# Kernel tuning notes

Measured on AMD Instinct MI355X. Metric: run time of the kernel, lower is better.

## Reference

```python
import jax, jax.numpy as jnp
import numpy as np

N = 30000      # input points
M = 7500       # sampled queries = floor(N * ratio), ratio=0.25
K = 16         # neighbors per query
D_X = 64       # input feature dim
D_REL = 64     # point_pos_nn output dim
D_F = D_X + D_REL  # fij_hat dim = 128


def setup_inputs() -> dict:
    key = jax.random.key(0)
    ks = jax.random.split(key, 6)
    x = jax.random.normal(ks[0], (N, D_X), jnp.float32)
    pos = jax.random.normal(ks[1], (N, 3), jnp.float32)
    idx = jax.random.randint(ks[2], (M,), 0, N)
    W_pos = jax.random.normal(ks[3], (10, D_REL), jnp.float32) / jnp.sqrt(10.0)
    b_pos = jnp.zeros((D_REL,), jnp.float32)
    W_att = jax.random.normal(ks[4], (D_F, D_F), jnp.float32) / jnp.sqrt(float(D_F))
    b_att = jnp.zeros((D_F,), jnp.float32)
    W_glob = jax.random.normal(ks[5], (D_F, D_F), jnp.float32) / jnp.sqrt(float(D_F))
    b_glob = jnp.zeros((D_F,), jnp.float32)
    return {"x": x, "pos": pos, "idx": idx, "W_pos": W_pos, "b_pos": b_pos,
            "W_att": W_att, "b_att": b_att, "W_glob": W_glob, "b_glob": b_glob}


def reference(x, pos, idx, W_pos, b_pos, W_att, b_att, W_glob, b_glob):
    # --- KNN: brute-force squared distances from sampled queries to all points ---
    pos_q = pos[idx]                                         # [M, 3]
    d2 = ((pos_q * pos_q).sum(-1)[:, None]
          + (pos * pos).sum(-1)[None, :]
          - 2.0 * pos_q @ pos.T)                             # [M, N]
    _, nbr = jax.lax.top_k(-d2, K)                           # [M, K] neighbor indices

    # --- Local Spatial Encoding (message) ---
    pos_j = pos[nbr]                                         # [M, K, 3]
    pos_i = jnp.broadcast_to(pos_q[:, None, :], pos_j.shape) # [M, K, 3]
    vij = pos_i - pos_j                                      # [M, K, 3]
    dij = jnp.linalg.norm(vij, axis=-1, keepdims=True)       # [M, K, 1]
    rel = jnp.concatenate([pos_i, pos_j, vij, dij], axis=-1) # [M, K, 10]
    rij = jax.nn.relu(rel @ W_pos + b_pos)                   # [M, K, D_REL]

    # --- Attentive pooling ---
    fij = jnp.concatenate([x[nbr], rij], axis=-1)            # [M, K, D_F]
    g = fij @ W_att + b_att                                  # [M, K, D_F]
    s = jax.nn.softmax(g, axis=-1)                           # softmax over feature dim
    aggr = jnp.mean(s * fij, axis=1)                         # mean over K neighbors -> [M, D_F]

    # --- global_nn (update) ---
    return jax.nn.relu(aggr @ W_glob + b_glob)               # [M, D_F]
```

## Files before the change

kernel.cpp:

```cpp
#include <hip/hip_runtime.h>
#include <stdint.h>

#define KNB   16
#define GD    64
#define GTOT  (GD * GD * GD)
#define GORIG (-6.5f)
#define GEDGE 0.203125f
#define GINV  (1.0f / GEDGE)
#define CAPW  640

typedef short short8 __attribute__((ext_vector_type(8)));
typedef float floatx4 __attribute__((ext_vector_type(4)));

__device__ __forceinline__ unsigned short f2bf(float x) {
  union { float f; uint32_t u; } v; v.f = x;
  uint32_t u = v.u + 0x7FFFu + ((v.u >> 16) & 1u);
  return (unsigned short)(u >> 16);
}
__device__ __forceinline__ float bf2f(unsigned short b) {
  return __uint_as_float(((uint32_t)b) << 16);
}
__device__ __forceinline__ int cellco(float v) {
  int c = (int)floorf((v - GORIG) * GINV);
  return c < 0 ? 0 : (c > GD - 1 ? GD - 1 : c);
}

__global__ void zero_kernel(int* __restrict__ count) {
  int i = (blockIdx.x * 256 + threadIdx.x) * 4;
  *(int4*)(count + i) = make_int4(0, 0, 0, 0);
}

__global__ void prep_kernel(const float* __restrict__ x,
                            const float* __restrict__ pos,
                            const float* __restrict__ W_att,
                            unsigned short* __restrict__ xb,
                            float4* __restrict__ pos4,
                            unsigned short* __restrict__ Wt,
                            int* __restrict__ ptcell,
                            int* __restrict__ count, int N) {
  int id = blockIdx.x * 256 + threadIdx.x;
  int nx8 = N * 8;
  if (id < nx8) {
    const float4* src = (const float4*)x + (size_t)id * 2;
    float4 a = src[0], b = src[1];
    short8 v;
    v[0] = (short)f2bf(a.x); v[1] = (short)f2bf(a.y);
    v[2] = (short)f2bf(a.z); v[3] = (short)f2bf(a.w);
    v[4] = (short)f2bf(b.x); v[5] = (short)f2bf(b.y);
    v[6] = (short)f2bf(b.z); v[7] = (short)f2bf(b.w);
    *(short8*)(xb + (size_t)id * 8) = v;
  } else if (id < nx8 + N) {
    int j = id - nx8;
    float px = pos[3 * j], py = pos[3 * j + 1], pz = pos[3 * j + 2];
    float pp = fmaf(px, px, fmaf(py, py, pz * pz));
    pos4[j] = make_float4(px, py, pz, pp);
    int cid = (cellco(pz) * GD + cellco(py)) * GD + cellco(px);
    ptcell[j] = cid;
    atomicAdd(&count[cid], 1);
  } else if (id < nx8 + N + 128 * 128) {
    int t = id - nx8 - N;
    int c = t >> 7, f = t & 127;
    Wt[f * 128 + c] = f2bf(W_att[t]);
  }
}

__global__ __launch_bounds__(256) void scan1(const int* __restrict__ count,
                                             int* __restrict__ partial) {
  int b = blockIdx.x, t = threadIdx.x;
  int v = count[b * 256 + t];
#pragma unroll
  for (int off = 1; off < 64; off <<= 1) v += __shfl_xor(v, off);
  __shared__ int ws_[4];
  if ((t & 63) == 0) ws_[t >> 6] = v;
  __syncthreads();
  if (t == 0) partial[b] = ws_[0] + ws_[1] + ws_[2] + ws_[3];
}

__global__ __launch_bounds__(256) void scan2(int* __restrict__ partial,
                                             int* __restrict__ cell_start) {
  int t = threadIdx.x;
  int v0 = partial[t * 4], v1 = partial[t * 4 + 1];
  int v2 = partial[t * 4 + 2], v3 = partial[t * 4 + 3];
  int s1 = v0 + v1, s2 = s1 + v2, s3 = s2 + v3;
  int x = s3;
  int lane = t & 63, wv = t >> 6;
#pragma unroll
  for (int off = 1; off < 64; off <<= 1) {
    int y = __shfl_up(x, off);
    if (lane >= off) x += y;
  }
  __shared__ int wsum[4];
  if (lane == 63) wsum[wv] = x;
  __syncthreads();
  int base = 0;
  for (int k = 0; k < wv; ++k) base += wsum[k];
  int excl = base + x - s3;
  partial[t * 4]     = excl;
  partial[t * 4 + 1] = excl + v0;
  partial[t * 4 + 2] = excl + s1;
  partial[t * 4 + 3] = excl + s2;
  if (t == 255) cell_start[GTOT] = excl + s3;
}

__global__ __launch_bounds__(256) void scan3(const int* __restrict__ count,
                                             const int* __restrict__ partial,
                                             int* __restrict__ cell_start,
                                             int* __restrict__ cursor) {
  int b = blockIdx.x, t = threadIdx.x;
  int v = count[b * 256 + t];
  int x = v;
  int lane = t & 63, wv = t >> 6;
#pragma unroll
  for (int off = 1; off < 64; off <<= 1) {
    int y = __shfl_up(x, off);
    if (lane >= off) x += y;
  }
  __shared__ int wsum[4];
  if (lane == 63) wsum[wv] = x;
  __syncthreads();
  int base = partial[b];
  for (int k = 0; k < wv; ++k) base += wsum[k];
  int excl = base + x - v;
  cell_start[b * 256 + t] = excl;
  cursor[b * 256 + t] = excl;
}

__global__ void scatter_kernel(const float4* __restrict__ pos4,
                               const int* __restrict__ ptcell,
                               int* __restrict__ cursor,
                               float4* __restrict__ spos4,
                               int* __restrict__ sid, int N) {
  int j = blockIdx.x * 256 + threadIdx.x;
  if (j >= N) return;
  int cid = ptcell[j];
  int slot = atomicAdd(&cursor[cid], 1);
  spos4[slot] = pos4[j];
  sid[slot] = j;
}

__global__ __launch_bounds__(256) void knn_grid(
    const float4* __restrict__ pos4, const float4* __restrict__ spos4,
    const int* __restrict__ sid, const int* __restrict__ cell_start,
    const int* __restrict__ idx, int* __restrict__ nbr, int M) {
  __shared__ unsigned long long cand[4][CAPW];
  __shared__ uint32_t rsA[4][64], rlA[4][64], rsB[4][64];
  __shared__ uint32_t rps[4][72];
  const int tid = threadIdx.x, wv = tid >> 6, ln = tid & 63;
  const int m = blockIdx.x * 4 + wv;
  if (m >= M) return;

  const float4 qp = pos4[idx[m]];
  const int cqx = cellco(qp.x), cqy = cellco(qp.y), cqz = cellco(qp.z);

  int tot = 0;
  unsigned long long taukey = ~0ull;
  bool done = false;
  for (int s = 1; s <= 64 && !done; ++s) {
    const int w = 2 * s + 1, npair = w * w;
    for (int base = 0; base < npair; base += 64) {
      int i = base + ln;
      int stA = 0, lA = 0, stB = 0, lB = 0;
      if (i < npair) {
        int dz = i / w - s, dy = i - (i / w) * w - s;
        int cz = cqz + dz, cy = cqy + dy;
        if (cz >= 0 && cz < GD && cy >= 0 && cy < GD) {
          int rowbase = (cz * GD + cy) * GD;
          int az = dz < 0 ? -dz : dz, ay = dy < 0 ? -dy : dy;
          int ch = az > ay ? az : ay;
          if (s == 1 || ch == s) {
            int x0 = cqx - s; if (x0 < 0) x0 = 0;
            int x1 = cqx + s; if (x1 > GD - 1) x1 = GD - 1;
            stA = cell_start[rowbase + x0];
            lA  = cell_start[rowbase + x1 + 1] - stA;
          } else {
            int xl = cqx - s, xr = cqx + s;
            if (xl >= 0) {
              stA = cell_start[rowbase + xl];
              lA  = cell_start[rowbase + xl + 1] - stA;
            }
            if (xr <= GD - 1) {
              stB = cell_start[rowbase + xr];
              lB  = cell_start[rowbase + xr + 1] - stB;
            }
          }
        }
      }
      int len = lA + lB;
      int xinc = len;
#pragma unroll
      for (int off = 1; off < 64; off <<= 1) {
        int y = __shfl_up(xinc, off);
        if (ln >= off) xinc += y;
      }
      int T = __shfl(xinc, 63);
      if (T == 0) continue;
      rps[wv][ln] = (uint32_t)(xinc - len);
      if (ln == 63) rps[wv][64] = (uint32_t)T;
      rsA[wv][ln] = (uint32_t)stA;
      rlA[wv][ln] = (uint32_t)lA;
      rsB[wv][ln] = (uint32_t)stB;

      for (int b2 = 0; b2 < T; b2 += 64) {
        if (tot + 64 > CAPW) {
          unsigned long long c[CAPW / 64];
#pragma unroll
          for (int chk = 0; chk < CAPW / 64; ++chk) {
            int slot = chk * 64 + ln;
            c[chk] = (slot < tot) ? cand[wv][slot] : ~0ull;
          }
          unsigned long long last = 0;
#pragma unroll
          for (int r = 0; r < KNB; ++r) {
            unsigned long long mn = c[0];
#pragma unroll
            for (int chk = 1; chk < CAPW / 64; ++chk)
              mn = (c[chk] < mn) ? c[chk] : mn;
#pragma unroll
            for (int off = 1; off < 64; off <<= 1) {
              unsigned long long o = __shfl_xor(mn, off);
              mn = (o < mn) ? o : mn;
            }
            if (ln == 0) cand[wv][r] = mn;
            last = mn;
#pragma unroll
            for (int chk = 0; chk < CAPW / 64; ++chk)
              if (c[chk] == mn) c[chk] = ~0ull;
          }
          tot = KNB;
          taukey = last;
        }
        int flat = b2 + ln;
        unsigned long long key = ~0ull;
        bool ok = false;
        if (flat < T) {
          int lo = 0;
#pragma unroll
          for (int step = 32; step > 0; step >>= 1) {
            int mid = lo + step;
            if (mid <= 63 && (int)rps[wv][mid] <= flat) lo = mid;
          }
          int o = flat - (int)rps[wv][lo];
          uint32_t sa = rsA[wv][lo], la = rlA[wv][lo];
          int p = (o < (int)la) ? (int)(sa + o)
                                : (int)(rsB[wv][lo] + (uint32_t)(o - (int)la));
          float4 pj = spos4[p];
          float dot = fmaf(qp.x, pj.x, fmaf(qp.y, pj.y, qp.z * pj.z));
          float tt  = fmaf(-2.f, dot, pj.w);
          float d2  = fmaxf(qp.w + tt, 0.f);
          key = ((unsigned long long)__float_as_uint(d2) << 32) |
                (uint32_t)sid[p];
          ok = key < taukey;
        }
        unsigned long long bm = __ballot(ok);
        int pos = __popcll(bm & ((1ull << ln) - 1ull));
        if (ok) cand[wv][tot + pos] = key;
        tot += __popcll(bm);
      }
    }
    if (tot >= KNB) {
      float fx = qp.x - GORIG, fy = qp.y - GORIG, fz = qp.z - GORIG;
      float r = 3.0e38f;
      if (cqx - s > 0)      r = fminf(r, fx - (float)(cqx - s) * GEDGE);
      if (cqx + s < GD - 1) r = fminf(r, (float)(cqx + s + 1) * GEDGE - fx);
      if (cqy - s > 0)      r = fminf(r, fy - (float)(cqy - s) * GEDGE);
      if (cqy + s < GD - 1) r = fminf(r, (float)(cqy + s + 1) * GEDGE - fy);
      if (cqz - s > 0)      r = fminf(r, fz - (float)(cqz - s) * GEDGE);
      if (cqz + s < GD - 1) r = fminf(r, (float)(cqz + s + 1) * GEDGE - fz);
      float r2 = (r > 1.0e19f) ? 3.0e38f : r * r;
      int cnt = 0;
      for (int chk = 0; chk * 64 < tot; ++chk) {
        int slot = chk * 64 + ln;
        unsigned long long key = cand[wv][slot];
        float d2v = __uint_as_float((uint32_t)(key >> 32));
        cnt += __popcll(__ballot(slot < tot && d2v <= r2));
      }
      if (cnt >= KNB) done = true;
    }
  }

  int nc = tot;
  unsigned long long c[CAPW / 64];
#pragma unroll
  for (int chk = 0; chk < CAPW / 64; ++chk) {
    int slot = chk * 64 + ln;
    unsigned long long k2 = cand[wv][slot];
    c[chk] = (slot < nc) ? k2 : ~0ull;
  }
#pragma unroll
  for (int r = 0; r < KNB; ++r) {
    unsigned long long mn = c[0];
#pragma unroll
    for (int chk = 1; chk < CAPW / 64; ++chk) mn = (c[chk] < mn) ? c[chk] : mn;
#pragma unroll
    for (int off = 1; off < 64; off <<= 1) {
      unsigned long long o = __shfl_xor(mn, off);
      mn = (o < mn) ? o : mn;
    }
    if (ln == 0) nbr[m * KNB + r] = (int)(uint32_t)mn;
#pragma unroll
    for (int chk = 0; chk < CAPW / 64; ++chk)
      if (c[chk] == mn) c[chk] = ~0ull;
  }
}

__global__ __launch_bounds__(256) void mid_kernel(
    const unsigned short* __restrict__ xb, const float4* __restrict__ pos4,
    const int* __restrict__ idx, const float* __restrict__ W_pos,
    const float* __restrict__ b_pos, const unsigned short* __restrict__ Wt,
    const float* __restrict__ b_att, const int* __restrict__ nbr,
    float* __restrict__ aggr, int M) {
  __shared__ __align__(16) unsigned short fijb[8][16][136];
  __shared__ int nbr_s[128];
  __shared__ float4 qpos_s[8];

  const int tid = threadIdx.x;
  const int wid = tid >> 6, lane = tid & 63;
  const int col = lane & 15, quad = lane >> 4;
  const int b = blockIdx.x;

  if (tid < 128) {
    int mq = b * 8 + (tid >> 4); if (mq >= M) mq = M - 1;
    nbr_s[tid] = nbr[mq * 16 + (tid & 15)];
  }
  if (tid < 8) {
    int mq = b * 8 + tid; if (mq >= M) mq = M - 1;
    qpos_s[tid] = pos4[idx[mq]];
  }
  float wp[10];
#pragma unroll
  for (int t = 0; t < 10; ++t) wp[t] = W_pos[t * 64 + lane];
  float bp = b_pos[lane];
  __syncthreads();

  {
    int rr = tid >> 1, h = tid & 1;
    int jn = nbr_s[rr];
    const short8* src = (const short8*)(xb + ((size_t)jn << 6) + (h << 5));
    short8 v0 = src[0], v1 = src[1], v2 = src[2], v3 = src[3];
    short8* dst = (short8*)&fijb[rr >> 4][rr & 15][h * 32];
    dst[0] = v0; dst[1] = v1; dst[2] = v2; dst[3] = v3;
  }
#pragma unroll
  for (int qi = 0; qi < 2; ++qi) {
    int q = wid * 2 + qi;
    float4 qp = qpos_s[q];
#pragma unroll 4
    for (int k = 0; k < 16; ++k) {
      int jn = nbr_s[q * 16 + k];
      float4 pj = pos4[jn];
      float vx = qp.x - pj.x, vy = qp.y - pj.y, vz = qp.z - pj.z;
      float dd = sqrtf(fmaf(vx, vx, fmaf(vy, vy, vz * vz)));
      float r = bp;
      r = fmaf(qp.x, wp[0], r); r = fmaf(qp.y, wp[1], r); r = fmaf(qp.z, wp[2], r);
      r = fmaf(pj.x, wp[3], r); r = fmaf(pj.y, wp[4], r); r = fmaf(pj.z, wp[5], r);
      r = fmaf(vx, wp[6], r);  r = fmaf(vy, wp[7], r);  r = fmaf(vz, wp[8], r);
      r = fmaf(dd, wp[9], r);
      r = fmaxf(r, 0.f);
      fijb[q][k][64 + lane] = f2bf(r);
    }
  }
  __syncthreads();

#pragma unroll 1
  for (int qi = 0; qi < 2; ++qi) {
    int q = wid * 2 + qi;
    int mq = b * 8 + q;

    short8 af[4];
#pragma unroll
    for (int cs = 0; cs < 4; ++cs)
      af[cs] = *(const short8*)&fijb[q][col][cs * 32 + quad * 8];

    floatx4 acc[8];
#pragma unroll
    for (int ft = 0; ft < 8; ++ft) {
      float bav = b_att[ft * 16 + col];
      floatx4 a = {bav, bav, bav, bav};
#pragma unroll
      for (int cs = 0; cs < 4; ++cs) {
        short8 bfrag =
            *(const short8*)&Wt[(ft * 16 + col) * 128 + cs * 32 + quad * 8];
        a = __builtin_amdgcn_mfma_f32_16x16x32_bf16(af[cs], bfrag, a, 0, 0, 0);
      }
      acc[ft] = a;
    }

    float rowmax[4], rowinv[4];
#pragma unroll
    for (int r = 0; r < 4; ++r) {
      float mx = acc[0][r];
#pragma unroll
      for (int ft = 1; ft < 8; ++ft) mx = fmaxf(mx, acc[ft][r]);
      mx = fmaxf(mx, __shfl_xor(mx, 1));
      mx = fmaxf(mx, __shfl_xor(mx, 2));
      mx = fmaxf(mx, __shfl_xor(mx, 4));
      mx = fmaxf(mx, __shfl_xor(mx, 8));
      float sm = 0.f;
#pragma unroll
      for (int ft = 0; ft < 8; ++ft) sm += __expf(acc[ft][r] - mx);
      sm += __shfl_xor(sm, 1);
      sm += __shfl_xor(sm, 2);
      sm += __shfl_xor(sm, 4);
      sm += __shfl_xor(sm, 8);
      rowmax[r] = mx;
      rowinv[r] = 1.0f / sm;
    }

#pragma unroll
    for (int ft = 0; ft < 8; ++ft) {
      float ap = 0.f;
#pragma unroll
      for (int r = 0; r < 4; ++r) {
        float s = __expf(acc[ft][r] - rowmax[r]) * rowinv[r];
        float fv = bf2f(fijb[q][quad * 4 + r][ft * 16 + col]);
        ap = fmaf(s, fv, ap);
      }
      ap += __shfl_xor(ap, 16);
      ap += __shfl_xor(ap, 32);
      if (quad == 0 && mq < M)
        aggr[mq * 128 + ft * 16 + col] = ap * (1.0f / 16.0f);
    }
  }
}

__global__ __launch_bounds__(256) void out_kernel(
    const float* __restrict__ aggr, const float* __restrict__ W_glob,
    const float* __restrict__ b_glob, float* __restrict__ out, int M) {
  __shared__ float ag[16][128];
  const int tid = threadIdx.x;
  const int mbase = blockIdx.x * 16;
  for (int s = tid; s < 16 * 128; s += 256) {
    int r = s >> 7, cc = s & 127;
    int m = mbase + r;
    ((float*)ag)[s] = (m < M) ? aggr[m * 128 + cc] : 0.0f;
  }
  __syncthreads();
  const int f = tid & 127, h = tid >> 7;
  float acc[8];
  float bg = b_glob[f];
#pragma unroll
  for (int i = 0; i < 8; ++i) acc[i] = bg;
  for (int c = 0; c < 128; c += 4) {
    float w0 = W_glob[(c + 0) * 128 + f];
    float w1 = W_glob[(c + 1) * 128 + f];
    float w2 = W_glob[(c + 2) * 128 + f];
    float w3 = W_glob[(c + 3) * 128 + f];
#pragma unroll
    for (int i = 0; i < 8; ++i) {
      const floatx4 a4 = *(const floatx4*)&ag[h * 8 + i][c];
      acc[i] += a4[0] * w0 + a4[1] * w1 + a4[2] * w2 + a4[3] * w3;
    }
  }
#pragma unroll
  for (int i = 0; i < 8; ++i) {
    int m = mbase + h * 8 + i;
    if (m < M) out[m * 128 + f] = fmaxf(acc[i], 0.0f);
  }
}

extern "C" void kernel_launch(void* const* d_in, const int* in_sizes, int n_in,
                              void* d_out, int out_size, void* d_ws,
                              size_t ws_size, hipStream_t stream) {
  const float* x      = (const float*)d_in[0];
  const float* pos    = (const float*)d_in[1];
  const int*   idx    = (const int*)d_in[2];
  const float* W_pos  = (const float*)d_in[3];
  const float* b_pos  = (const float*)d_in[4];
  const float* W_att  = (const float*)d_in[5];
  const float* b_att  = (const float*)d_in[6];
  const float* W_glob = (const float*)d_in[7];
  const float* b_glob = (const float*)d_in[8];
  float* out = (float*)d_out;

  const int N = in_sizes[1] / 3;
  const int M = in_sizes[2];

  char* ws = (char*)d_ws;
  size_t o = 0;
  float4* pos4 = (float4*)(ws + o);               o += ((size_t)N * 16 + 255) & ~(size_t)255;
  unsigned short* xb = (unsigned short*)(ws + o); o += ((size_t)N * 128 + 255) & ~(size_t)255;
  unsigned short* Wt = (unsigned short*)(ws + o); o += (128 * 128 * 2 + 255) & ~(size_t)255;
  int* nbr = (int*)(ws + o);                      o += (((size_t)M * KNB * 4) + 255) & ~(size_t)255;
  int* ptcell = (int*)(ws + o);                   o += (((size_t)N * 4) + 255) & ~(size_t)255;
  int* count = (int*)(ws + o);                    o += ((size_t)GTOT * 4 + 255) & ~(size_t)255;
  int* cursor = (int*)(ws + o);                   o += ((size_t)GTOT * 4 + 255) & ~(size_t)255;
  int* cell_start = (int*)(ws + o);               o += ((size_t)(GTOT + 1) * 4 + 255) & ~(size_t)255;
  int* partial = (int*)(ws + o);                  o += (1024 * 4 + 255) & ~(size_t)255;
  float4* spos4 = (float4*)(ws + o);              o += ((size_t)N * 16 + 255) & ~(size_t)255;
  int* sid = (int*)(ws + o);                      o += (((size_t)N * 4) + 255) & ~(size_t)255;
  float* aggr = (float*)(ws + o);                 o += ((size_t)M * 128 * 4 + 255) & ~(size_t)255;

  zero_kernel<<<GTOT / 1024, 256, 0, stream>>>(count);

  int prep_ids = N * 8 + N + 128 * 128;
  prep_kernel<<<(prep_ids + 255) / 256, 256, 0, stream>>>(
      x, pos, W_att, xb, pos4, Wt, ptcell, count, N);

  scan1<<<GTOT / 256, 256, 0, stream>>>(count, partial);
  scan2<<<1, 256, 0, stream>>>(partial, cell_start);
  scan3<<<GTOT / 256, 256, 0, stream>>>(count, partial, cell_start, cursor);

  scatter_kernel<<<(N + 255) / 256, 256, 0, stream>>>(pos4, ptcell, cursor,
                                                      spos4, sid, N);

  knn_grid<<<(M + 3) / 4, 256, 0, stream>>>(pos4, spos4, sid, cell_start, idx,
                                            nbr, M);

  mid_kernel<<<(M + 7) / 8, 256, 0, stream>>>(xb, pos4, idx, W_pos, b_pos, Wt,
                                              b_att, nbr, aggr, M);
  out_kernel<<<(M + 15) / 16, 256, 0, stream>>>(aggr, W_glob, b_glob, out, M);
}
```

Before: 202.3 us.

## Grow KNN grid search shells geometrically instead of one ring at a time

The KNN cell search now expands its search cube by doubling the radius (1,2,4,...,63) rather than adding one ring per iteration. Each step scans only the shell between the previous and new radius, with rows clipped to the grid bounds. This cuts the number of shell iterations, prefix scans and termination checks per query. In exchange it can pull in more candidates than needed at once, which may overflow the candidate buffer more often and trigger extra compaction passes.

Result: slower. 266.7 us (+31.9%).

```diff
diff --git a/kernel.cpp b/kernel.cpp
--- a/kernel.cpp
+++ b/kernel.cpp
@@ -154,34 +154,43 @@
 
   int tot = 0;
   unsigned long long taukey = ~0ull;
+  int s_lo = -1;
   bool done = false;
-  for (int s = 1; s <= 64 && !done; ++s) {
-    const int w = 2 * s + 1, npair = w * w;
+  for (int si = 0; si < 7 && !done; ++si) {
+    const int s = (si == 6) ? 63 : (1 << si);
+    const int z0 = (cqz - s < 0) ? 0 : cqz - s;
+    const int z1 = (cqz + s > GD - 1) ? GD - 1 : cqz + s;
+    const int y0 = (cqy - s < 0) ? 0 : cqy - s;
+    const int y1 = (cqy + s > GD - 1) ? GD - 1 : cqy + s;
+    const int wy = y1 - y0 + 1;
+    const int npair = (z1 - z0 + 1) * wy;
     for (int base = 0; base < npair; base += 64) {
       int i = base + ln;
       int stA = 0, lA = 0, stB = 0, lB = 0;
       if (i < npair) {
-        int dz = i / w - s, dy = i - (i / w) * w - s;
-        int cz = cqz + dz, cy = cqy + dy;
-        if (cz >= 0 && cz < GD && cy >= 0 && cy < GD) {
-          int rowbase = (cz * GD + cy) * GD;
-          int az = dz < 0 ? -dz : dz, ay = dy < 0 ? -dy : dy;
-          int ch = az > ay ? az : ay;
-          if (s == 1 || ch == s) {
-            int x0 = cqx - s; if (x0 < 0) x0 = 0;
-            int x1 = cqx + s; if (x1 > GD - 1) x1 = GD - 1;
-            stA = cell_start[rowbase + x0];
-            lA  = cell_start[rowbase + x1 + 1] - stA;
-          } else {
-            int xl = cqx - s, xr = cqx + s;
-            if (xl >= 0) {
-              stA = cell_start[rowbase + xl];
-              lA  = cell_start[rowbase + xl + 1] - stA;
-            }
-            if (xr <= GD - 1) {
-              stB = cell_start[rowbase + xr];
-              lB  = cell_start[rowbase + xr + 1] - stB;
-            }
+        int zz = z0 + i / wy;
+        int yy = y0 + (i - (i / wy) * wy);
+        int dz = zz - cqz, dy = yy - cqy;
+        int az = dz < 0 ? -dz : dz, ay = dy < 0 ? -dy : dy;
+        int ch = az > ay ? az : ay;
+        int rowbase = (zz * GD + yy) * GD;
+        if (ch > s_lo) {
+          int x0 = cqx - s; if (x0 < 0) x0 = 0;
+          int x1 = cqx + s; if (x1 > GD - 1) x1 = GD - 1;
+          stA = cell_start[rowbase + x0];
+          lA  = cell_start[rowbase + x1 + 1] - stA;
+        } else {
+          int xl0 = cqx - s; if (xl0 < 0) xl0 = 0;
+          int xl1 = cqx - s_lo - 1;
+          if (xl1 >= xl0) {
+            stA = cell_start[rowbase + xl0];
+            lA  = cell_start[rowbase + xl1 + 1] - stA;
+          }
+          int xr0 = cqx + s_lo + 1;
+          int xr1 = cqx + s; if (xr1 > GD - 1) xr1 = GD - 1;
+          if (xr1 >= xr0) {
+            stB = cell_start[rowbase + xr0];
+            lB  = cell_start[rowbase + xr1 + 1] - stB;
           }
         }
       }
@@ -195,7 +204,6 @@
       int T = __shfl(xinc, 63);
       if (T == 0) continue;
       rps[wv][ln] = (uint32_t)(xinc - len);
-      if (ln == 63) rps[wv][64] = (uint32_t)T;
       rsA[wv][ln] = (uint32_t)stA;
       rlA[wv][ln] = (uint32_t)lA;
       rsB[wv][ln] = (uint32_t)stB;
@@ -276,6 +284,7 @@
       }
       if (cnt >= KNB) done = true;
     }
+    s_lo = s;
   }
 
   int nc = tot;
```
